# Kernel tuning notes

Hardware: AMD Instinct MI355X
Metric: run time of the kernel (lower is better)

## Reference

```python
import jax, jax.numpy as jnp
import numpy as np

N = 50000      # nodes
E = 800000     # edges
M = 1000000    # total subgraph membership rows
D = 128        # atom_fea_len
ED = 64        # nbr_fea_len
H = 8          # heads
C = D // H     # per-head dim


def _ln(x, g, b, eps=1e-5):
    mu = x.mean(-1, keepdims=True)
    var = ((x - mu) ** 2).mean(-1, keepdims=True)
    return (x - mu) / jnp.sqrt(var + eps) * g + b


def setup_inputs() -> dict:
    key = jax.random.key(0)
    ks = jax.random.split(key, 16)
    s = 0.05
    inp = {
        "x": jax.random.normal(ks[0], (N, D), jnp.float32),
        "edge_index": jax.random.randint(ks[1], (2, E), 0, N, jnp.int32),
        "edge_attr": jax.random.normal(ks[2], (E, ED), jnp.float32),
        "sub_nodes": jax.random.randint(ks[3], (M,), 0, N, jnp.int32),
        "sub_indicator": jax.random.randint(ks[4], (M,), 0, N, jnp.int32),
        # TransformerConv params (PyG: lin_query/key/value, lin_edge, lin_skip, all with bias)
        "Wq": jax.random.normal(ks[5], (D, D), jnp.float32) * s,
        "bq": jnp.zeros((D,), jnp.float32),
        "Wk": jax.random.normal(ks[6], (D, D), jnp.float32) * s,
        "bk": jnp.zeros((D,), jnp.float32),
        "Wv": jax.random.normal(ks[7], (D, D), jnp.float32) * s,
        "bv": jnp.zeros((D,), jnp.float32),
        "We": jax.random.normal(ks[8], (ED, D), jnp.float32) * s,
        "be": jnp.zeros((D,), jnp.float32),
        "Ws": jax.random.normal(ks[9], (D, D), jnp.float32) * s,
        "bs": jnp.zeros((D,), jnp.float32),
        # subgraph_norm
        "sn_g": jnp.ones((D,), jnp.float32),
        "sn_b": jnp.zeros((D,), jnp.float32),
        # subgraph_proj: Linear -> SiLU -> Linear
        "p1_w": jax.random.normal(ks[10], (D, D), jnp.float32) * s,
        "p1_b": jnp.zeros((D,), jnp.float32),
        "p2_w": jax.random.normal(ks[11], (D, D), jnp.float32) * s,
        "p2_b": jnp.zeros((D,), jnp.float32),
        # out_norm
        "on_g": jnp.ones((D,), jnp.float32),
        "on_b": jnp.zeros((D,), jnp.float32),
    }
    return inp


def reference(x, edge_index, edge_attr, sub_nodes, sub_indicator,
              Wq, bq, Wk, bk, Wv, bv, We, be, Ws, bs,
              sn_g, sn_b, p1_w, p1_b, p2_w, p2_b, on_g, on_b):
    n = x.shape[0]
    src, dst = edge_index[0], edge_index[1]  # messages flow src -> dst (PyG source_to_target)

    # ---- TransformerConv ----
    q = (x @ Wq + bq).reshape(n, H, C)
    k = (x @ Wk + bk).reshape(n, H, C)
    v = (x @ Wv + bv).reshape(n, H, C)
    e = (edge_attr @ We + be).reshape(-1, H, C)       # [E,H,C]
    ke = k[src] + e                                    # edge-conditioned keys
    ve = v[src] + e                                    # edge-conditioned values
    alpha = (q[dst] * ke).sum(-1) / jnp.sqrt(jnp.asarray(C, x.dtype))  # [E,H]
    # scatter-softmax over incoming edges of each dst node
    m = jax.ops.segment_max(alpha, dst, num_segments=n)               # [N,H]
    ea = jnp.exp(alpha - m[dst])
    denom = jax.ops.segment_sum(ea, dst, num_segments=n)              # [N,H]
    num = jax.ops.segment_sum(ea[:, :, None] * ve, dst, num_segments=n)  # [N,H,C]
    attn = num / jnp.where(denom > 0, denom, 1.0)[:, :, None]
    x_trans = attn.reshape(n, H * C) + (x @ Ws + bs)   # concat heads + root skip

    # ---- subgraph branch: gather -> LayerNorm -> MLP -> scatter-mean ----
    sx = x[sub_nodes]                                  # [M,D]
    sx = _ln(sx, sn_g, sn_b)
    sx = jax.nn.silu(sx @ p1_w + p1_b) @ p2_w + p2_b
    cnt = jax.ops.segment_sum(jnp.ones((sx.shape[0],), x.dtype), sub_indicator, num_segments=n)
    sub_x = jax.ops.segment_sum(sx, sub_indicator, num_segments=n) / jnp.maximum(cnt, 1.0)[:, None]

    # ---- combine (dropout is identity in eval) ----
    out = _ln(x + x_trans + sub_x, on_g, on_b)
    return jax.nn.silu(out)
```

## Files before the change

### kernel.cpp

```cpp
#include <hip/hip_runtime.h>
#include <math.h>

#define DD 128
#define EDD 64

typedef __attribute__((ext_vector_type(8))) short bf16x8;
typedef __attribute__((ext_vector_type(4))) float f32x4;

__device__ inline unsigned short f2bf(float f) {
    unsigned int u = __float_as_uint(f);
    u += 0x7FFFu + ((u >> 16) & 1u);
    return (unsigned short)(u >> 16);
}
__device__ inline unsigned int pack2bf16(float lo, float hi) {
    return (unsigned int)f2bf(lo) | ((unsigned int)f2bf(hi) << 16);
}
__device__ inline float bflo(unsigned int u) { return __uint_as_float(u << 16); }
__device__ inline float bfhi(unsigned int u) { return __uint_as_float(u & 0xffff0000u); }

__global__ __launch_bounds__(256) void packw_kernel(const float* __restrict__ w,
                                                    unsigned short* __restrict__ packed)
{
    int idx = blockIdx.x * 256 + threadIdx.x;
    if (idx >= DD * DD) return;
    int j    = idx & 7;
    int lane = (idx >> 3) & 63;
    int kt   = (idx >> 9) & 3;
    int ncf  = idx >> 11;
    int kk  = kt * 32 + (lane >> 4) * 8 + j;
    int col = ncf * 16 + (lane & 15);
    packed[idx] = f2bf(w[kk * DD + col]);
}

__device__ inline void gemm_b(const bf16x8 af[4][2], const unsigned short* __restrict__ packB,
                              int wc, int lane, f32x4 acc[2][4])
{
    #pragma unroll
    for (int i = 0; i < 2; i++)
        #pragma unroll
        for (int j = 0; j < 4; j++) acc[i][j] = (f32x4){0.f, 0.f, 0.f, 0.f};
    #pragma unroll
    for (int kt = 0; kt < 4; kt++) {
        #pragma unroll
        for (int nc = 0; nc < 4; nc++) {
            bf16x8 b = *(const bf16x8*)&packB[(((wc * 4 + nc) * 4 + kt) * 64 + lane) * 8];
            acc[0][nc] = __builtin_amdgcn_mfma_f32_16x16x32_bf16(af[kt][0], b, acc[0][nc], 0, 0, 0);
            acc[1][nc] = __builtin_amdgcn_mfma_f32_16x16x32_bf16(af[kt][1], b, acc[1][nc], 0, 0, 0);
        }
    }
}

__global__ __launch_bounds__(256, 4) void lin4_mfma_kernel(
    const float* __restrict__ x,
    const unsigned short* __restrict__ packBq, const float* __restrict__ bq,
    const unsigned short* __restrict__ packBk, const float* __restrict__ bk,
    const unsigned short* __restrict__ packBv, const float* __restrict__ bv,
    const unsigned short* __restrict__ packBs, const float* __restrict__ bs,
    const float* __restrict__ sn_g, const float* __restrict__ sn_b,
    float* __restrict__ q, float* __restrict__ kvbuf, float* __restrict__ pre,
    unsigned int* __restrict__ lnx, int N)
{
    __shared__ unsigned short sxs[64 * DD];
    int tid = threadIdx.x;
    int lane = tid & 63, wid = tid >> 6;
    size_t m0 = (size_t)blockIdx.x * 64;

    {
        float g0 = sn_g[2 * lane], g1 = sn_g[2 * lane + 1];
        float b0 = sn_b[2 * lane], b1 = sn_b[2 * lane + 1];
        #pragma unroll
        for (int r = 0; r < 16; r++) {
            int tr = wid * 16 + r;
            size_t row = m0 + tr;
            float v0 = 0.f, v1 = 0.f;
            if (row < (size_t)N) {
                float2 xv = *(const float2*)&x[row * DD + 2 * lane];
                v0 = xv.x; v1 = xv.y;
            }
            unsigned int uidx = ((unsigned)(tr * 64 + lane)) ^ (((unsigned)tr & 7u) << 2);
            ((unsigned int*)sxs)[uidx] = pack2bf16(v0, v1);
            float s1 = v0 + v1, s2 = v0 * v0 + v1 * v1;
            #pragma unroll
            for (int o = 32; o >= 1; o >>= 1) { s1 += __shfl_xor(s1, o); s2 += __shfl_xor(s2, o); }
            float mean = s1 * (1.f / DD);
            float var  = s2 * (1.f / DD) - mean * mean;
            float rs = rsqrtf(var + 1e-5f);
            if (row < (size_t)N)
                lnx[row * 64 + lane] = pack2bf16((v0 - mean) * rs * g0 + b0,
                                                 (v1 - mean) * rs * g1 + b1);
        }
    }
    __syncthreads();

    int wr = wid >> 1, wc = wid & 1;
    int rA = wr * 32 + (lane & 15);
    int kb = (lane >> 4) * 8;

    bf16x8 af[4][2];
    #pragma unroll
    for (int kt = 0; kt < 4; kt++) {
        int k0 = kt * 32 + kb;
        af[kt][0] = *(const bf16x8*)&sxs[((rA)      * DD + k0) ^ ((rA & 7) << 3)];
        int rA1 = rA + 16;
        af[kt][1] = *(const bf16x8*)&sxs[((rA1)     * DD + k0) ^ ((rA1 & 7) << 3)];
    }

    f32x4 acc[2][4];
    int colb = wc * 64 + (lane & 15);
    int jrow = (lane >> 4) * 4;

    gemm_b(af, packBq, wc, lane, acc);
    #pragma unroll
    for (int mrf = 0; mrf < 2; mrf++) {
        int rbase = wr * 32 + mrf * 16 + jrow;
        #pragma unroll
        for (int nc = 0; nc < 4; nc++) {
            int col = colb + nc * 16;
            float bias = bq[col];
            #pragma unroll
            for (int j = 0; j < 4; j++) {
                size_t row = m0 + rbase + j;
                if (row < (size_t)N) q[row * DD + col] = acc[mrf][nc][j] + bias;
            }
        }
    }
    gemm_b(af, packBk, wc, lane, acc);
    #pragma unroll
    for (int mrf = 0; mrf < 2; mrf++) {
        int rbase = wr * 32 + mrf * 16 + jrow;
        #pragma unroll
        for (int nc = 0; nc < 4; nc++) {
            int col = colb + nc * 16;
            int slot = ((col >> 1) << 2) + (col & 1);
            float bias = bk[col];
            #pragma unroll
            for (int j = 0; j < 4; j++) {
                size_t row = m0 + rbase + j;
                if (row < (size_t)N) kvbuf[row * 256 + slot] = acc[mrf][nc][j] + bias;
            }
        }
    }
    gemm_b(af, packBv, wc, lane, acc);
    #pragma unroll
    for (int mrf = 0; mrf < 2; mrf++) {
        int rbase = wr * 32 + mrf * 16 + jrow;
        #pragma unroll
        for (int nc = 0; nc < 4; nc++) {
            int col = colb + nc * 16;
            int slot = ((col >> 1) << 2) + (col & 1) + 2;
            float bias = bv[col];
            #pragma unroll
            for (int j = 0; j < 4; j++) {
                size_t row = m0 + rbase + j;
                if (row < (size_t)N) kvbuf[row * 256 + slot] = acc[mrf][nc][j] + bias;
            }
        }
    }
    gemm_b(af, packBs, wc, lane, acc);
    #pragma unroll
    for (int mrf = 0; mrf < 2; mrf++) {
        int rbase = wr * 32 + mrf * 16 + jrow;
        #pragma unroll
        for (int nc = 0; nc < 4; nc++) {
            int col = colb + nc * 16;
            float bias = bs[col];
            #pragma unroll
            for (int j = 0; j < 4; j++) {
                size_t row = m0 + rbase + j;
                if (row < (size_t)N)
                    pre[row * DD + col] = x[row * DD + col] + acc[mrf][nc][j] + bias;
            }
        }
    }
}

__global__ __launch_bounds__(256, 4) void mlpnode_kernel(
    const unsigned int* __restrict__ lnx,
    const unsigned short* __restrict__ packB1, const float* __restrict__ p1b,
    const unsigned short* __restrict__ packB2, const float* __restrict__ p2b,
    unsigned short* __restrict__ fnode, int N)
{
    __shared__ unsigned short sxs[64 * DD];
    int tid = threadIdx.x;
    int lane = tid & 63, wid = tid >> 6;
    size_t m0 = (size_t)blockIdx.x * 64;

    #pragma unroll
    for (int r = 0; r < 16; r++) {
        int tr = wid * 16 + r;
        size_t row = m0 + tr;
        unsigned int val = (row < (size_t)N) ? lnx[row * 64 + lane] : 0u;
        unsigned int uidx = ((unsigned)(tr * 64 + lane)) ^ (((unsigned)tr & 7u) << 2);
        ((unsigned int*)sxs)[uidx] = val;
    }
    __syncthreads();

    int wr = wid >> 1, wc = wid & 1;
    int rA = wr * 32 + (lane & 15);
    int kb = (lane >> 4) * 8;

    f32x4 acc[2][4];
    #pragma unroll
    for (int i = 0; i < 2; i++)
        #pragma unroll
        for (int j = 0; j < 4; j++) acc[i][j] = (f32x4){0.f, 0.f, 0.f, 0.f};
    #pragma unroll
    for (int kt = 0; kt < 4; kt++) {
        int k0 = kt * 32 + kb;
        bf16x8 a0 = *(const bf16x8*)&sxs[((rA)  * DD + k0) ^ ((rA & 7) << 3)];
        int rA1 = rA + 16;
        bf16x8 a1 = *(const bf16x8*)&sxs[((rA1) * DD + k0) ^ ((rA1 & 7) << 3)];
        #pragma unroll
        for (int nc = 0; nc < 4; nc++) {
            bf16x8 b = *(const bf16x8*)&packB1[(((wc * 4 + nc) * 4 + kt) * 64 + lane) * 8];
            acc[0][nc] = __builtin_amdgcn_mfma_f32_16x16x32_bf16(a0, b, acc[0][nc], 0, 0, 0);
            acc[1][nc] = __builtin_amdgcn_mfma_f32_16x16x32_bf16(a1, b, acc[1][nc], 0, 0, 0);
        }
    }
    __syncthreads();

    {
        float bias1[4];
        #pragma unroll
        for (int nc = 0; nc < 4; nc++) bias1[nc] = p1b[wc * 64 + nc * 16 + (lane & 15)];
        #pragma unroll
        for (int mrf = 0; mrf < 2; mrf++) {
            int rbase = wr * 32 + mrf * 16 + (lane >> 4) * 4;
            #pragma unroll
            for (int nc = 0; nc < 4; nc++) {
                int col = wc * 64 + nc * 16 + (lane & 15);
                #pragma unroll
                for (int j = 0; j < 4; j++) {
                    float h = acc[mrf][nc][j] + bias1[nc];
                    h = h / (1.f + __expf(-h));
                    int rr = rbase + j;
                    sxs[(rr * DD + col) ^ ((rr & 7) << 3)] = f2bf(h);
                }
            }
        }
    }
    __syncthreads();

    f32x4 acc2[2][4];
    #pragma unroll
    for (int i = 0; i < 2; i++)
        #pragma unroll
        for (int j = 0; j < 4; j++) acc2[i][j] = (f32x4){0.f, 0.f, 0.f, 0.f};
    #pragma unroll
    for (int kt = 0; kt < 4; kt++) {
        int k0 = kt * 32 + kb;
        bf16x8 a0 = *(const bf16x8*)&sxs[((rA)  * DD + k0) ^ ((rA & 7) << 3)];
        int rA1 = rA + 16;
        bf16x8 a1 = *(const bf16x8*)&sxs[((rA1) * DD + k0) ^ ((rA1 & 7) << 3)];
        #pragma unroll
        for (int nc = 0; nc < 4; nc++) {
            bf16x8 b = *(const bf16x8*)&packB2[(((wc * 4 + nc) * 4 + kt) * 64 + lane) * 8];
            acc2[0][nc] = __builtin_amdgcn_mfma_f32_16x16x32_bf16(a0, b, acc2[0][nc], 0, 0, 0);
            acc2[1][nc] = __builtin_amdgcn_mfma_f32_16x16x32_bf16(a1, b, acc2[1][nc], 0, 0, 0);
        }
    }

    {
        float bias2[4];
        #pragma unroll
        for (int nc = 0; nc < 4; nc++) bias2[nc] = p2b[wc * 64 + nc * 16 + (lane & 15)];
        #pragma unroll
        for (int mrf = 0; mrf < 2; mrf++) {
            int rbase = wr * 32 + mrf * 16 + (lane >> 4) * 4;
            #pragma unroll
            for (int nc = 0; nc < 4; nc++) {
                int col = wc * 64 + nc * 16 + (lane & 15);
                #pragma unroll
                for (int j = 0; j < 4; j++) {
                    size_t row = m0 + rbase + j;
                    if (row < (size_t)N)
                        fnode[row * DD + col] = f2bf(acc2[mrf][nc][j] + bias2[nc]);
                }
            }
        }
    }
}

__global__ void count_kernel(const int* __restrict__ idx, int n, int* __restrict__ cnt)
{
    int i = blockIdx.x * blockDim.x + threadIdx.x;
    int stride = gridDim.x * blockDim.x;
    for (; i < n; i += stride) atomicAdd(&cnt[idx[i]], 1);
}

__global__ __launch_bounds__(1024) void bscan_kernel(
    const int* __restrict__ inA, const int* __restrict__ inB,
    int* __restrict__ exA, int* __restrict__ exB,
    int* __restrict__ bsA, int* __restrict__ bsB, int N)
{
    const int* in = blockIdx.y ? inB : inA;
    int* ex = blockIdx.y ? exB : exA;
    int* bs = blockIdx.y ? bsB : bsA;
    __shared__ int s[1024];
    int tid = threadIdx.x;
    int i = blockIdx.x * 1024 + tid;
    int val = (i < N) ? in[i] : 0;
    s[tid] = val; __syncthreads();
    for (int off = 1; off < 1024; off <<= 1) {
        int t = (tid >= off) ? s[tid - off] : 0;
        __syncthreads();
        s[tid] += t;
        __syncthreads();
    }
    if (i < N) ex[i] = s[tid] - val;
    if (tid == 1023) bs[blockIdx.x] = s[1023];
}

__global__ void bsum_kernel(int* __restrict__ bsA, int* __restrict__ bsB,
                            int* __restrict__ indptrA, int* __restrict__ indptrB,
                            int nb, int N)
{
    int which = threadIdx.x;
    if (which < 2) {
        int* bs = which ? bsB : bsA;
        int* indptr = which ? indptrB : indptrA;
        int run = 0;
        for (int b = 0; b < nb; b++) { int v = bs[b]; bs[b] = run; run += v; }
        indptr[N] = run;
    }
}

__global__ void bfix_kernel(int* __restrict__ exA, int* __restrict__ fillA, const int* __restrict__ bsA,
                            int* __restrict__ exB, int* __restrict__ fillB, const int* __restrict__ bsB,
                            int N)
{
    int i = blockIdx.x * blockDim.x + threadIdx.x;
    if (i < N) {
        int vA = exA[i] + bsA[i >> 10];
        exA[i] = vA; fillA[i] = vA;
        int vB = exB[i] + bsB[i >> 10];
        exB[i] = vB; fillB[i] = vB;
    }
}

__global__ void escatter_kernel(const int* __restrict__ srcA, const int* __restrict__ dstA, int E,
                                int* __restrict__ fill, int2* __restrict__ spair)
{
    int i = blockIdx.x * blockDim.x + threadIdx.x;
    int stride = gridDim.x * blockDim.x;
    for (; i < E; i += stride) {
        int d = dstA[i];
        int pos = atomicAdd(&fill[d], 1);
        spair[pos] = make_int2(srcA[i], i);
    }
}

__global__ void sscatter_kernel(const int* __restrict__ sub_nodes, const int* __restrict__ sub_ind,
                                int M, int* __restrict__ sfill, int* __restrict__ snode)
{
    int i = blockIdx.x * blockDim.x + threadIdx.x;
    int stride = gridDim.x * blockDim.x;
    for (; i < M; i += stride) {
        int seg = sub_ind[i];
        int pos = atomicAdd(&sfill[seg], 1);
        snode[pos] = sub_nodes[i];
    }
}

__global__ __launch_bounds__(256) void qprep_kernel(
    const float* __restrict__ q, const float* __restrict__ We,
    unsigned int* __restrict__ qweU, int N)
{
    int tid = threadIdx.x;
    int wave = tid >> 6, lane = tid & 63;
    int n = blockIdx.x * 4 + wave;
    if (n >= N) return;
    int jj = lane & 7, g = lane >> 3;
    int hc0 = g * 16;
    const float4* qp = (const float4*)&q[(size_t)n * DD + hc0];
    float4 q0 = qp[0], q1 = qp[1], q2 = qp[2], q3 = qp[3];
    float qWe[8];
    #pragma unroll
    for (int r = 0; r < 8; r++) {
        const float4* wp = (const float4*)&We[(size_t)(8 * jj + r) * DD + hc0];
        float4 wa = wp[0], wb = wp[1], wc = wp[2], wd = wp[3];
        qWe[r] = q0.x * wa.x + q0.y * wa.y + q0.z * wa.z + q0.w * wa.w
               + q1.x * wb.x + q1.y * wb.y + q1.z * wb.z + q1.w * wb.w
               + q2.x * wc.x + q2.y * wc.y + q2.z * wc.z + q2.w * wc.w
               + q3.x * wd.x + q3.y * wd.y + q3.z * wd.z + q3.w * wd.w;
    }
    uint4 packed;
    packed.x = pack2bf16(qWe[0], qWe[1]);
    packed.y = pack2bf16(qWe[2], qWe[3]);
    packed.z = pack2bf16(qWe[4], qWe[5]);
    packed.w = pack2bf16(qWe[6], qWe[7]);
    *(uint4*)&qweU[(size_t)n * 256 + 4 * lane] = packed;
}

__global__ __launch_bounds__(256, 4) void attn_kernel(
    const float* __restrict__ q, const float* __restrict__ kvbuf,
    const float* __restrict__ edge_attr, const unsigned int* __restrict__ qweU,
    const float* __restrict__ We, const float* __restrict__ be,
    const int* __restrict__ indptr, const int2* __restrict__ spair,
    float* __restrict__ pre, int N)
{
    int tid = threadIdx.x;
    int wave = tid >> 6, lane = tid & 63;
    int n = blockIdx.x * 4 + wave;
    if (n >= N) return;

    int gbase = lane & 56;
    int jj = lane & 7;
    int c0 = lane * 2;

    float2 qv  = *(const float2*)&q[(size_t)n * DD + c0];
    float2 bev = *(const float2*)&be[c0];

    float t = qv.x * bev.x + qv.y * bev.y;
    t += __shfl_xor(t, 1); t += __shfl_xor(t, 2); t += __shfl_xor(t, 4);
    float qbe4 = t * 0.25f;

    uint4 qw = *(const uint4*)&qweU[(size_t)n * 256 + 4 * lane];
    float qwe0 = bflo(qw.x), qwe1 = bfhi(qw.x), qwe2 = bflo(qw.y), qwe3 = bfhi(qw.y);
    float qwe4 = bflo(qw.z), qwe5 = bfhi(qw.z), qwe6 = bflo(qw.w), qwe7 = bfhi(qw.w);

    int start = indptr[n], end = indptr[n + 1];
    float s = 0.f, av0 = 0.f, av1 = 0.f;
    float aea[8];
    #pragma unroll
    for (int r = 0; r < 8; r++) aea[r] = 0.f;

    int ii = start;
    for (; ii + 3 < end; ii += 4) {
        int2 se[4];
        #pragma unroll
        for (int u = 0; u < 4; u++) se[u] = spair[ii + u];
        float4 ea0[4], ea1[4], kv[4];
        #pragma unroll
        for (int u = 0; u < 4; u++) {
            const float4* eap = (const float4*)&edge_attr[(size_t)se[u].y * EDD + 8 * jj];
            ea0[u] = eap[0];
            ea1[u] = eap[1];
            kv[u] = *(const float4*)&kvbuf[(size_t)se[u].x * 256 + 4 * lane];
        }
        float p[4];
        #pragma unroll
        for (int u = 0; u < 4; u++) {
            float part = qv.x * kv[u].x + qv.y * kv[u].y
                       + ea0[u].x * qwe0 + ea0[u].y * qwe1 + ea0[u].z * qwe2 + ea0[u].w * qwe3
                       + ea1[u].x * qwe4 + ea1[u].y * qwe5 + ea1[u].z * qwe6 + ea1[u].w * qwe7;
            part += __shfl_xor(part, 1);
            part += __shfl_xor(part, 2);
            part += __shfl_xor(part, 4);
            p[u] = __expf(part * 0.25f + qbe4);
        }
        #pragma unroll
        for (int u = 0; u < 4; u++) {
            s += p[u];
            av0 += p[u] * kv[u].z;
            av1 += p[u] * kv[u].w;
            aea[0] += p[u] * ea0[u].x; aea[1] += p[u] * ea0[u].y;
            aea[2] += p[u] * ea0[u].z; aea[3] += p[u] * ea0[u].w;
            aea[4] += p[u] * ea1[u].x; aea[5] += p[u] * ea1[u].y;
            aea[6] += p[u] * ea1[u].z; aea[7] += p[u] * ea1[u].w;
        }
    }
    for (; ii < end; ii++) {
        int2 se = spair[ii];
        const float4* eap = (const float4*)&edge_attr[(size_t)se.y * EDD + 8 * jj];
        float4 ea0 = eap[0];
        float4 ea1 = eap[1];
        float4 kv = *(const float4*)&kvbuf[(size_t)se.x * 256 + 4 * lane];
        float part = qv.x * kv.x + qv.y * kv.y
                   + ea0.x * qwe0 + ea0.y * qwe1 + ea0.z * qwe2 + ea0.w * qwe3
                   + ea1.x * qwe4 + ea1.y * qwe5 + ea1.z * qwe6 + ea1.w * qwe7;
        part += __shfl_xor(part, 1);
        part += __shfl_xor(part, 2);
        part += __shfl_xor(part, 4);
        float p = __expf(part * 0.25f + qbe4);
        s += p;
        av0 += p * kv.z;
        av1 += p * kv.w;
        aea[0] += p * ea0.x; aea[1] += p * ea0.y; aea[2] += p * ea0.z; aea[3] += p * ea0.w;
        aea[4] += p * ea1.x; aea[5] += p * ea1.y; aea[6] += p * ea1.z; aea[7] += p * ea1.w;
    }

    if (end > start) {
        float inv = 1.f / s;
        float oe0 = 0.f, oe1 = 0.f;
        #pragma unroll
        for (int m = 0; m < 8; m++) {
            #pragma unroll
            for (int r = 0; r < 8; r++) {
                float a = __shfl(aea[r], gbase + m);
                float2 w = *(const float2*)&We[(size_t)(8 * m + r) * DD + c0];
                oe0 += a * w.x;
                oe1 += a * w.y;
            }
        }
        size_t o = (size_t)n * DD + c0;
        pre[o]     += (av0 + oe0) * inv + bev.x;
        pre[o + 1] += (av1 + oe1) * inv + bev.y;
    }
}

__global__ __launch_bounds__(256) void final2_kernel(
    const float* __restrict__ pre, const unsigned int* __restrict__ fnodeU,
    const int* __restrict__ sindptr, const int* __restrict__ snode,
    const float* __restrict__ on_g, const float* __restrict__ on_b,
    float* __restrict__ out, int N)
{
    int tid = threadIdx.x;
    int wave = tid >> 6, lane = tid & 63;
    int n = blockIdx.x * 4 + wave;
    if (n >= N) return;
    int c0 = 2 * lane;

    int start = sindptr[n], end = sindptr[n + 1];
    float sum0 = 0.f, sum1 = 0.f;
    int ii = start;
    for (; ii + 3 < end; ii += 4) {
        int n0 = snode[ii], n1 = snode[ii + 1], n2 = snode[ii + 2], n3 = snode[ii + 3];
        unsigned int u0 = fnodeU[(size_t)n0 * 64 + lane];
        unsigned int u1 = fnodeU[(size_t)n1 * 64 + lane];
        unsigned int u2 = fnodeU[(size_t)n2 * 64 + lane];
        unsigned int u3 = fnodeU[(size_t)n3 * 64 + lane];
        sum0 += bflo(u0) + bflo(u1) + bflo(u2) + bflo(u3);
        sum1 += bfhi(u0) + bfhi(u1) + bfhi(u2) + bfhi(u3);
    }
    for (; ii < end; ii++) {
        unsigned int u = fnodeU[(size_t)snode[ii] * 64 + lane];
        sum0 += bflo(u);
        sum1 += bfhi(u);
    }
    float inv = 1.f / fmaxf((float)(end - start), 1.f);

    float2 pv = *(const float2*)&pre[(size_t)n * DD + c0];
    float v0 = pv.x + sum0 * inv;
    float v1 = pv.y + sum1 * inv;

    float s1 = v0 + v1, s2 = v0 * v0 + v1 * v1;
    #pragma unroll
    for (int off = 32; off >= 1; off >>= 1) { s1 += __shfl_xor(s1, off); s2 += __shfl_xor(s2, off); }
    float mean = s1 * (1.f / DD);
    float var  = s2 * (1.f / DD) - mean * mean;
    float rs = rsqrtf(var + 1e-5f);

    float2 gv = *(const float2*)&on_g[c0];
    float2 bv = *(const float2*)&on_b[c0];
    float ov0 = (v0 - mean) * rs * gv.x + bv.x;
    float ov1 = (v1 - mean) * rs * gv.y + bv.y;
    float2 res;
    res.x = ov0 / (1.f + __expf(-ov0));
    res.y = ov1 / (1.f + __expf(-ov1));
    *(float2*)&out[(size_t)n * DD + c0] = res;
}

extern "C" void kernel_launch(void* const* d_in, const int* in_sizes, int n_in,
                              void* d_out, int out_size, void* d_ws, size_t ws_size,
                              hipStream_t stream)
{
    const float* x         = (const float*)d_in[0];
    const int*   edge_index= (const int*)  d_in[1];
    const float* edge_attr = (const float*)d_in[2];
    const int*   sub_nodes = (const int*)  d_in[3];
    const int*   sub_ind   = (const int*)  d_in[4];
    const float* Wq = (const float*)d_in[5];  const float* bq = (const float*)d_in[6];
    const float* Wk = (const float*)d_in[7];  const float* bk = (const float*)d_in[8];
    const float* Wv = (const float*)d_in[9];  const float* bv = (const float*)d_in[10];
    const float* We = (const float*)d_in[11]; const float* be = (const float*)d_in[12];
    const float* Ws = (const float*)d_in[13]; const float* bs = (const float*)d_in[14];
    const float* sn_g = (const float*)d_in[15]; const float* sn_b = (const float*)d_in[16];
    const float* p1w = (const float*)d_in[17]; const float* p1b = (const float*)d_in[18];
    const float* p2w = (const float*)d_in[19]; const float* p2b = (const float*)d_in[20];
    const float* on_g = (const float*)d_in[21]; const float* on_b = (const float*)d_in[22];

    int N = in_sizes[0] / DD;
    int E = in_sizes[1] / 2;
    int M = in_sizes[3];
    float* out = (float*)d_out;

    unsigned short* packB1 = (unsigned short*)d_ws;
    unsigned short* packB2 = packB1 + DD * DD;
    unsigned short* packBq = packB2 + DD * DD;
    unsigned short* packBk = packBq + DD * DD;
    unsigned short* packBv = packBk + DD * DD;
    unsigned short* packBs = packBv + DD * DD;
    size_t ND = (size_t)N * DD;
    float* q     = (float*)(packBs + DD * DD);
    float* kvbuf = q + ND;
    float* pre   = kvbuf + 2 * ND;
    unsigned int* qweU  = (unsigned int*)(pre + ND);
    unsigned int* lnx   = qweU + (size_t)N * 256;
    unsigned int* fnode = lnx + (size_t)N * 64;
    int2* spair  = (int2*)(fnode + (size_t)N * 64);
    int* indptr  = (int*)(spair + E);
    int* fill    = indptr + (N + 1);
    int* deg     = fill + N;
    int* cnt     = deg + N;
    int* sindptr = cnt + N;
    int* sfill   = sindptr + (N + 1);
    int* snode   = sfill + N;
    int* bsA     = snode + M;
    int* bsB     = bsA + 64;

    const int* srcA = edge_index;
    const int* dstA = edge_index + E;

    int nb = (N + 1023) / 1024;

    hipMemsetAsync(deg, 0, (size_t)N * sizeof(int), stream);
    hipMemsetAsync(cnt, 0, (size_t)N * sizeof(int), stream);

    packw_kernel<<<64, 256, 0, stream>>>(p1w, packB1);
    packw_kernel<<<64, 256, 0, stream>>>(p2w, packB2);
    packw_kernel<<<64, 256, 0, stream>>>(Wq, packBq);
    packw_kernel<<<64, 256, 0, stream>>>(Wk, packBk);
    packw_kernel<<<64, 256, 0, stream>>>(Wv, packBv);
    packw_kernel<<<64, 256, 0, stream>>>(Ws, packBs);

    lin4_mfma_kernel<<<(N + 63) / 64, 256, 0, stream>>>(x, packBq, bq, packBk, bk, packBv, bv,
                                                        packBs, bs, sn_g, sn_b,
                                                        q, kvbuf, pre, lnx, N);
    mlpnode_kernel<<<(N + 63) / 64, 256, 0, stream>>>(lnx, packB1, p1b, packB2, p2b,
                                                      (unsigned short*)fnode, N);
    count_kernel<<<2048, 256, 0, stream>>>(dstA, E, deg);
    count_kernel<<<2048, 256, 0, stream>>>(sub_ind, M, cnt);
    {
        dim3 g(nb, 2);
        bscan_kernel<<<g, 1024, 0, stream>>>(deg, cnt, indptr, sindptr, bsA, bsB, N);
    }
    bsum_kernel<<<1, 64, 0, stream>>>(bsA, bsB, indptr, sindptr, nb, N);
    bfix_kernel<<<(N + 255) / 256, 256, 0, stream>>>(indptr, fill, bsA, sindptr, sfill, bsB, N);
    escatter_kernel<<<2048, 256, 0, stream>>>(srcA, dstA, E, fill, spair);
    sscatter_kernel<<<2048, 256, 0, stream>>>(sub_nodes, sub_ind, M, sfill, snode);
    qprep_kernel<<<(N + 3) / 4, 256, 0, stream>>>(q, We, qweU, N);
    attn_kernel<<<(N + 3) / 4, 256, 0, stream>>>(q, kvbuf, edge_attr, qweU, We, be,
                                                 indptr, spair, pre, N);
    final2_kernel<<<(N + 3) / 4, 256, 0, stream>>>(pre, fnode, sindptr, snode, on_g, on_b, out, N);
}
```

Measured before the change: 797.5 us.

## Store K/V in bf16 planes and pre-gather edge_attr into CSR-ordered bf16

The linear kernel now writes K and V as separate bf16 planes instead of an interleaved fp32 buffer. A new kernel gathers edge_attr into destination-sorted order and converts it to bf16, so the attention loop reads it contiguously at half the bytes. The aim is to cut gather traffic in the memory-bound attention kernel. In exchange it adds an extra pass over edge_attr (read fp32, write bf16) and loses some precision in K, V and edge features.

```diff
diff --git a/kernel.cpp b/kernel.cpp
--- a/kernel.cpp
+++ b/kernel.cpp
@@ -57,8 +57,8 @@
     const unsigned short* __restrict__ packBv, const float* __restrict__ bv,
     const unsigned short* __restrict__ packBs, const float* __restrict__ bs,
     const float* __restrict__ sn_g, const float* __restrict__ sn_b,
-    float* __restrict__ q, float* __restrict__ kvbuf, float* __restrict__ pre,
-    unsigned int* __restrict__ lnx, int N)
+    float* __restrict__ q, unsigned short* __restrict__ kplane, unsigned short* __restrict__ vplane,
+    float* __restrict__ pre, unsigned int* __restrict__ lnx, int N)
 {
     __shared__ unsigned short sxs[64 * DD];
     int tid = threadIdx.x;
@@ -131,12 +131,11 @@
         #pragma unroll
         for (int nc = 0; nc < 4; nc++) {
             int col = colb + nc * 16;
-            int slot = ((col >> 1) << 2) + (col & 1);
             float bias = bk[col];
             #pragma unroll
             for (int j = 0; j < 4; j++) {
                 size_t row = m0 + rbase + j;
-                if (row < (size_t)N) kvbuf[row * 256 + slot] = acc[mrf][nc][j] + bias;
+                if (row < (size_t)N) kplane[row * DD + col] = f2bf(acc[mrf][nc][j] + bias);
             }
         }
     }
@@ -147,12 +146,11 @@
         #pragma unroll
         for (int nc = 0; nc < 4; nc++) {
             int col = colb + nc * 16;
-            int slot = ((col >> 1) << 2) + (col & 1) + 2;
             float bias = bv[col];
             #pragma unroll
             for (int j = 0; j < 4; j++) {
                 size_t row = m0 + rbase + j;
-                if (row < (size_t)N) kvbuf[row * 256 + slot] = acc[mrf][nc][j] + bias;
+                if (row < (size_t)N) vplane[row * DD + col] = f2bf(acc[mrf][nc][j] + bias);
             }
         }
     }
@@ -350,6 +348,26 @@
     }
 }
 
+__global__ __launch_bounds__(256) void egather_kernel(
+    const float* __restrict__ edge_attr, const int2* __restrict__ spair,
+    unsigned int* __restrict__ ea16u, int E)
+{
+    size_t i = (size_t)blockIdx.x * blockDim.x + threadIdx.x;
+    size_t stride = (size_t)gridDim.x * blockDim.x;
+    size_t total = (size_t)E * 8;
+    for (; i < total; i += stride) {
+        size_t pos = i >> 3;
+        int part = (int)(i & 7);
+        int eid = spair[pos].y;
+        const float4* s = (const float4*)&edge_attr[(size_t)eid * EDD + part * 8];
+        float4 a = s[0], b = s[1];
+        uint4 o;
+        o.x = pack2bf16(a.x, a.y); o.y = pack2bf16(a.z, a.w);
+        o.z = pack2bf16(b.x, b.y); o.w = pack2bf16(b.z, b.w);
+        *(uint4*)&ea16u[pos * 32 + part * 4] = o;
+    }
+}
+
 __global__ void sscatter_kernel(const int* __restrict__ sub_nodes, const int* __restrict__ sub_ind,
                                 int M, int* __restrict__ sfill, int* __restrict__ snode)
 {
@@ -393,8 +411,9 @@
 }
 
 __global__ __launch_bounds__(256, 4) void attn_kernel(
-    const float* __restrict__ q, const float* __restrict__ kvbuf,
-    const float* __restrict__ edge_attr, const unsigned int* __restrict__ qweU,
+    const float* __restrict__ q,
+    const unsigned int* __restrict__ kplane32, const unsigned int* __restrict__ vplane32,
+    const unsigned int* __restrict__ ea16u, const unsigned int* __restrict__ qweU,
     const float* __restrict__ We, const float* __restrict__ be,
     const int* __restrict__ indptr, const int2* __restrict__ spair,
     float* __restrict__ pre, int N)
@@ -430,20 +449,22 @@
         int2 se[4];
         #pragma unroll
         for (int u = 0; u < 4; u++) se[u] = spair[ii + u];
-        float4 ea0[4], ea1[4], kv[4];
+        uint4 ea[4];
+        unsigned int ku[4], vu[4];
         #pragma unroll
         for (int u = 0; u < 4; u++) {
-            const float4* eap = (const float4*)&edge_attr[(size_t)se[u].y * EDD + 8 * jj];
-            ea0[u] = eap[0];
-            ea1[u] = eap[1];
-            kv[u] = *(const float4*)&kvbuf[(size_t)se[u].x * 256 + 4 * lane];
+            ea[u] = *(const uint4*)&ea16u[(size_t)(ii + u) * 32 + jj * 4];
+            ku[u] = kplane32[(size_t)se[u].x * 64 + lane];
+            vu[u] = vplane32[(size_t)se[u].x * 64 + lane];
         }
         float p[4];
         #pragma unroll
         for (int u = 0; u < 4; u++) {
-            float part = qv.x * kv[u].x + qv.y * kv[u].y
-                       + ea0[u].x * qwe0 + ea0[u].y * qwe1 + ea0[u].z * qwe2 + ea0[u].w * qwe3
-                       + ea1[u].x * qwe4 + ea1[u].y * qwe5 + ea1[u].z * qwe6 + ea1[u].w * qwe7;
+            float part = qv.x * bflo(ku[u]) + qv.y * bfhi(ku[u])
+                       + bflo(ea[u].x) * qwe0 + bfhi(ea[u].x) * qwe1
+                       + bflo(ea[u].y) * qwe2 + bfhi(ea[u].y) * qwe3
+                       + bflo(ea[u].z) * qwe4 + bfhi(ea[u].z) * qwe5
+                       + bflo(ea[u].w) * qwe6 + bfhi(ea[u].w) * qwe7;
             part += __shfl_xor(part, 1);
             part += __shfl_xor(part, 2);
             part += __shfl_xor(part, 4);
@@ -452,32 +473,35 @@
         #pragma unroll
         for (int u = 0; u < 4; u++) {
             s += p[u];
-            av0 += p[u] * kv[u].z;
-            av1 += p[u] * kv[u].w;
-            aea[0] += p[u] * ea0[u].x; aea[1] += p[u] * ea0[u].y;
-            aea[2] += p[u] * ea0[u].z; aea[3] += p[u] * ea0[u].w;
-            aea[4] += p[u] * ea1[u].x; aea[5] += p[u] * ea1[u].y;
-            aea[6] += p[u] * ea1[u].z; aea[7] += p[u] * ea1[u].w;
+            av0 += p[u] * bflo(vu[u]);
+            av1 += p[u] * bfhi(vu[u]);
+            aea[0] += p[u] * bflo(ea[u].x); aea[1] += p[u] * bfhi(ea[u].x);
+            aea[2] += p[u] * bflo(ea[u].y); aea[3] += p[u] * bfhi(ea[u].y);
+            aea[4] += p[u] * bflo(ea[u].z); aea[5] += p[u] * bfhi(ea[u].z);
+            aea[6] += p[u] * bflo(ea[u].w); aea[7] += p[u] * bfhi(ea[u].w);
         }
     }
     for (; ii < end; ii++) {
         int2 se = spair[ii];
-        const float4* eap = (const float4*)&edge_attr[(size_t)se.y * EDD + 8 * jj];
-        float4 ea0 = eap[0];
-        float4 ea1 = eap[1];
-        float4 kv = *(const float4*)&kvbuf[(size_t)se.x * 256 + 4 * lane];
-        float part = qv.x * kv.x + qv.y * kv.y
-                   + ea0.x * qwe0 + ea0.y * qwe1 + ea0.z * qwe2 + ea0.w * qwe3
-                   + ea1.x * qwe4 + ea1.y * qwe5 + ea1.z * qwe6 + ea1.w * qwe7;
+        uint4 ea = *(const uint4*)&ea16u[(size_t)ii * 32 + jj * 4];
+        unsigned int ku = kplane32[(size_t)se.x * 64 + lane];
+        unsigned int vu = vplane32[(size_t)se.x * 64 + lane];
+        float part = qv.x * bflo(ku) + qv.y * bfhi(ku)
+                   + bflo(ea.x) * qwe0 + bfhi(ea.x) * qwe1
+                   + bflo(ea.y) * qwe2 + bfhi(ea.y) * qwe3
+                   + bflo(ea.z) * qwe4 + bfhi(ea.z) * qwe5
+                   + bflo(ea.w) * qwe6 + bfhi(ea.w) * qwe7;
         part += __shfl_xor(part, 1);
         part += __shfl_xor(part, 2);
         part += __shfl_xor(part, 4);
         float p = __expf(part * 0.25f + qbe4);
         s += p;
-        av0 += p * kv.z;
-        av1 += p * kv.w;
-        aea[0] += p * ea0.x; aea[1] += p * ea0.y; aea[2] += p * ea0.z; aea[3] += p * ea0.w;
-        aea[4] += p * ea1.x; aea[5] += p * ea1.y; aea[6] += p * ea1.z; aea[7] += p * ea1.w;
+        av0 += p * bflo(vu);
+        av1 += p * bfhi(vu);
+        aea[0] += p * bflo(ea.x); aea[1] += p * bfhi(ea.x);
+        aea[2] += p * bflo(ea.y); aea[3] += p * bfhi(ea.y);
+        aea[4] += p * bflo(ea.z); aea[5] += p * bfhi(ea.z);
+        aea[6] += p * bflo(ea.w); aea[7] += p * bfhi(ea.w);
     }
 
     if (end > start) {
@@ -583,12 +607,14 @@
     unsigned short* packBs = packBv + DD * DD;
     size_t ND = (size_t)N * DD;
     float* q     = (float*)(packBs + DD * DD);
-    float* kvbuf = q + ND;
-    float* pre   = kvbuf + 2 * ND;
+    unsigned short* kplane = (unsigned short*)(q + ND);
+    unsigned short* vplane = kplane + ND;
+    float* pre   = (float*)(vplane + ND);
     unsigned int* qweU  = (unsigned int*)(pre + ND);
     unsigned int* lnx   = qweU + (size_t)N * 256;
     unsigned int* fnode = lnx + (size_t)N * 64;
-    int2* spair  = (int2*)(fnode + (size_t)N * 64);
+    unsigned int* ea16u = fnode + (size_t)N * 64;
+    int2* spair  = (int2*)(ea16u + (size_t)E * 32);
     int* indptr  = (int*)(spair + E);
     int* fill    = indptr + (N + 1);
     int* deg     = fill + N;
@@ -616,7 +642,7 @@
 
     lin4_mfma_kernel<<<(N + 63) / 64, 256, 0, stream>>>(x, packBq, bq, packBk, bk, packBv, bv,
                                                         packBs, bs, sn_g, sn_b,
-                                                        q, kvbuf, pre, lnx, N);
+                                                        q, kplane, vplane, pre, lnx, N);
     mlpnode_kernel<<<(N + 63) / 64, 256, 0, stream>>>(lnx, packB1, p1b, packB2, p2b,
                                                       (unsigned short*)fnode, N);
     count_kernel<<<2048, 256, 0, stream>>>(dstA, E, deg);
@@ -628,9 +654,11 @@
     bsum_kernel<<<1, 64, 0, stream>>>(bsA, bsB, indptr, sindptr, nb, N);
     bfix_kernel<<<(N + 255) / 256, 256, 0, stream>>>(indptr, fill, bsA, sindptr, sfill, bsB, N);
     escatter_kernel<<<2048, 256, 0, stream>>>(srcA, dstA, E, fill, spair);
+    egather_kernel<<<4096, 256, 0, stream>>>(edge_attr, spair, ea16u, E);
     sscatter_kernel<<<2048, 256, 0, stream>>>(sub_nodes, sub_ind, M, sfill, snode);
     qprep_kernel<<<(N + 3) / 4, 256, 0, stream>>>(q, We, qweU, N);
-    attn_kernel<<<(N + 3) / 4, 256, 0, stream>>>(q, kvbuf, edge_attr, qweU, We, be,
-                                                 indptr, spair, pre, N);
+    attn_kernel<<<(N + 3) / 4, 256, 0, stream>>>(q, (const unsigned int*)kplane,
+                                                 (const unsigned int*)vplane, ea16u, qweU,
+                                                 We, be, indptr, spair, pre, N);
     final2_kernel<<<(N + 3) / 4, 256, 0, stream>>>(pre, fnode, sindptr, snode, on_g, on_b, out, N);
 }
```

Measured after the change: 805.8 us. About the same (+1.0%).
